# Kernel optimization log

Measured on AMD Instinct MI355X. Metric: run time of the kernel, lower is better.

Reference implementation:

```python
import jax, jax.numpy as jnp
import numpy as np

D_MODEL = 1024
N_HEAD = 16
N_HEAD_MOE = 8
N_EXPERTS = 8
TOP_N = 2
CAP_FACTOR = 1.25
THRESHOLD = 0.2
BAL_COEF = 0.01
Z_COEF = 0.001
B, S = 8, 1024


def setup_inputs() -> dict:
    key = jax.random.key(0)
    ks = jax.random.split(key, 12)
    d, E = D_MODEL, N_EXPERTS
    w = lambda k, shape: jax.random.normal(k, shape, jnp.float32) * 0.02
    return {
        "x": jax.random.normal(ks[0], (B, S, d), jnp.float32),
        "Wq": w(ks[1], (d, d)), "Wk": w(ks[2], (d, d)), "Wv": w(ks[3], (d, d)), "Wo": w(ks[4], (d, d)),
        "bq": jnp.zeros((d,), jnp.float32), "bk": jnp.zeros((d,), jnp.float32),
        "bv": jnp.zeros((d,), jnp.float32), "bo": jnp.zeros((d,), jnp.float32),
        "ln1_g": jnp.ones((d,), jnp.float32), "ln1_b": jnp.zeros((d,), jnp.float32),
        "ln2_g": jnp.ones((d,), jnp.float32), "ln2_b": jnp.zeros((d,), jnp.float32),
        "gate_W": w(ks[5], (d, E)),
        "eWq": w(ks[6], (E, d, d)), "eWk": w(ks[7], (E, d, d)),
        "eWv": w(ks[8], (E, d, d)), "eWo": w(ks[9], (E, d, d)),
    }


def _layernorm(x, g, b, eps=1e-5):
    mu = jnp.mean(x, -1, keepdims=True)
    var = jnp.var(x, -1, keepdims=True)
    return (x - mu) * jax.lax.rsqrt(var + eps) * g + b


def _mha(x, Wq, Wk, Wv, bq, bk, bv, Wo, bo):
    b, s, d = x.shape
    h, hd = N_HEAD, d // N_HEAD
    q = (x @ Wq + bq).reshape(b, s, h, hd)
    k = (x @ Wk + bk).reshape(b, s, h, hd)
    v = (x @ Wv + bv).reshape(b, s, h, hd)
    att = jax.nn.softmax(jnp.einsum('bqhd,bkhd->bhqk', q, k) * (hd ** -0.5), axis=-1)
    o = jnp.einsum('bhqk,bkhd->bqhd', att, v).reshape(b, s, d)
    return o @ Wo + bo


def _moe(x, gate_W, eWq, eWk, eWv, eWo):
    # ST-MoE style top-n routing with capacity dropping; experts are self-attention blocks.
    b, s, d = x.shape
    E = N_EXPERTS
    C = int(S * TOP_N * CAP_FACTOR / E)  # per-expert capacity (per batch row)
    logits = x @ gate_W                      # [b,s,E]
    z_loss = jnp.mean(jnp.square(jax.nn.logsumexp(logits, axis=-1)))
    probs = jax.nn.softmax(logits, axis=-1)
    gates, idxs = jax.lax.top_k(probs, TOP_N)  # [b,s,TOP_N]
    # load-balance loss: E * sum_e (top-1 dispatch fraction) * (mean router prob)
    f = jnp.mean(jax.nn.one_hot(idxs[..., 0], E, dtype=x.dtype), axis=(0, 1))
    P = jnp.mean(probs, axis=(0, 1))
    balance_loss = E * jnp.sum(f * P)

    bb = jnp.broadcast_to(jnp.arange(b)[:, None], (b, s))
    counts = jnp.zeros((b, E), jnp.int32)
    expert_in = jnp.zeros((E, b, C, d), x.dtype)
    slots = []
    for k in range(TOP_N):  # small fixed loop over routing slots
        e_idx = idxs[..., k]
        g = gates[..., k]
        keep_thr = (g > THRESHOLD) if k > 0 else jnp.ones(g.shape, dtype=bool)
        oh = jax.nn.one_hot(e_idx, E, dtype=jnp.int32) * keep_thr[..., None].astype(jnp.int32)
        # exclusive running position within each (batch, expert) buffer
        pos_all = jnp.cumsum(oh, axis=1) - oh + counts[:, None, :]
        pos = jnp.take_along_axis(pos_all, e_idx[..., None], axis=2)[..., 0]
        counts = counts + jnp.sum(oh, axis=1)
        keep = keep_thr & (pos < C)
        p = jnp.clip(pos, 0, C - 1)
        expert_in = expert_in.at[e_idx, bb, p].add(x * keep[..., None].astype(x.dtype))
        slots.append((e_idx, p, keep, g))

    # each expert: multi-head self-attention over its C capacity slots
    h, hd = N_HEAD_MOE, d // N_HEAD_MOE
    q = jnp.einsum('ebcd,edf->ebcf', expert_in, eWq).reshape(E, b, C, h, hd)
    kk = jnp.einsum('ebcd,edf->ebcf', expert_in, eWk).reshape(E, b, C, h, hd)
    v = jnp.einsum('ebcd,edf->ebcf', expert_in, eWv).reshape(E, b, C, h, hd)
    att = jax.nn.softmax(jnp.einsum('ebqhd,ebkhd->ebhqk', q, kk) * (hd ** -0.5), axis=-1)
    o = jnp.einsum('ebhqk,ebkhd->ebqhd', att, v).reshape(E, b, C, d)
    expert_out = jnp.einsum('ebcd,edf->ebcf', o, eWo)

    # combine: gather each token's slot output, weighted by its gate
    y = jnp.zeros_like(x)
    for e_idx, p, keep, g in slots:
        y = y + expert_out[e_idx, bb, p] * (g * keep.astype(x.dtype))[..., None]
    bal = BAL_COEF * balance_loss
    zl = Z_COEF * z_loss
    return y, bal + zl, bal, zl


def reference(x, Wq, Wk, Wv, Wo, bq, bk, bv, bo, ln1_g, ln1_b, ln2_g, ln2_b,
              gate_W, eWq, eWk, eWv, eWo):
    attn = _mha(x, Wq, Wk, Wv, bq, bk, bv, Wo, bo)
    x1 = _layernorm(x + attn, ln1_g, ln1_b)
    moe_out, aux, bal, zl = _moe(x1, gate_W, eWq, eWk, eWv, eWo)
    out = _layernorm(x1 + moe_out, ln2_g, ln2_b)
    return (out, aux, bal, zl)
```

## Files before the change

### kernel.cpp

```cpp
#include <hip/hip_runtime.h>
#include <hip/hip_bf16.h>
#include <math.h>

#define DM    1024
#define NH1   16
#define HDIM1 64
#define NH2   8
#define HDIM2 128
#define NE    8
#define CAPE  320
#define BATCH 8
#define SEQ   1024
#define NTOK  (BATCH*SEQ)
#define OUTN  ((long)NTOK*DM)
#define ECB   ((long)BATCH*CAPE*DM)

typedef short bf16x8 __attribute__((ext_vector_type(8)));
typedef float f32x4  __attribute__((ext_vector_type(4)));

__device__ __forceinline__ unsigned short f2bf(float f) {
    __hip_bfloat16 h = __float2bfloat16(f);
    return *reinterpret_cast<unsigned short*>(&h);
}
__device__ __forceinline__ float bf2f(unsigned short u) {
    unsigned int x = ((unsigned int)u) << 16;
    return __builtin_bit_cast(float, x);
}

__device__ __forceinline__ void async16(const void* g, void* lds) {
    __builtin_amdgcn_global_load_lds(
        (const __attribute__((address_space(1))) unsigned int*)g,
        (__attribute__((address_space(3))) unsigned int*)lds, 16, 0, 0);
}

__device__ __forceinline__ void gemm_core(
    const unsigned short* __restrict__ A, const unsigned short* __restrict__ Bt,
    int m0, int n0, int K, short* ldsA, short* ldsB, f32x4 (&acc)[4][4])
{
    const int t    = threadIdx.x;
    const int lane = t & 63, w = t >> 6;
    const int wr = w >> 1, wc = w & 1;
    const int lq = lane >> 4, lm = lane & 15;
    const int srow = w*16 + (lane >> 2);
    const int skc  = (lane & 3) * 8;
    for (int kb = 0; kb < K; kb += 32) {
        #pragma unroll
        for (int p = 0; p < 2; ++p) {
            async16(A  + (size_t)(m0 + srow + p*64)*K + kb + skc,
                    &ldsA[(w*16 + p*64)*32]);
            async16(Bt + (size_t)(n0 + srow + p*64)*K + kb + skc,
                    &ldsB[(w*16 + p*64)*32]);
        }
        __syncthreads();
        bf16x8 aF[4], bF[4];
        #pragma unroll
        for (int i = 0; i < 4; ++i)
            aF[i] = *(const bf16x8*)&ldsA[(wr*64 + i*16 + lm)*32 + lq*8];
        #pragma unroll
        for (int j = 0; j < 4; ++j)
            bF[j] = *(const bf16x8*)&ldsB[(wc*64 + j*16 + lm)*32 + lq*8];
        #pragma unroll
        for (int i = 0; i < 4; ++i)
            #pragma unroll
            for (int j = 0; j < 4; ++j)
                acc[i][j] = __builtin_amdgcn_mfma_f32_16x16x32_bf16(aF[i], bF[j], acc[i][j], 0, 0, 0);
        __syncthreads();
    }
}

__global__ __launch_bounds__(256) void gemm_bt_f32(
    const unsigned short* __restrict__ A, const unsigned short* __restrict__ Bt,
    const float* __restrict__ bias, float* __restrict__ C, int N, int K)
{
    __shared__ short ldsA[128*32];
    __shared__ short ldsB[128*32];
    const int lane = threadIdx.x & 63, w = threadIdx.x >> 6;
    const int wr = w >> 1, wc = w & 1;
    const int lq = lane >> 4, lm = lane & 15;
    const int m0 = blockIdx.y * 128, n0 = blockIdx.x * 128;
    f32x4 acc[4][4];
    #pragma unroll
    for (int i = 0; i < 4; ++i)
        #pragma unroll
        for (int j = 0; j < 4; ++j) acc[i][j] = (f32x4){0.f,0.f,0.f,0.f};
    gemm_core(A, Bt, m0, n0, K, ldsA, ldsB, acc);
    #pragma unroll
    for (int j = 0; j < 4; ++j) {
        const int gcol = n0 + wc*64 + j*16 + lm;
        const float badd = bias ? bias[gcol] : 0.f;
        #pragma unroll
        for (int i = 0; i < 4; ++i) {
            const int grow = m0 + wr*64 + i*16 + lq*4;
            #pragma unroll
            for (int r = 0; r < 4; ++r)
                C[(size_t)(grow + r)*N + gcol] = acc[i][j][r] + badd;
        }
    }
}

__global__ __launch_bounds__(256) void gemm_qkv(
    const unsigned short* __restrict__ A, const unsigned short* __restrict__ Bt,
    const float* __restrict__ bq, const float* __restrict__ bk, const float* __restrict__ bv,
    unsigned short* __restrict__ C)
{
    __shared__ short ldsA[128*32];
    __shared__ short ldsB[128*32];
    const int lane = threadIdx.x & 63, w = threadIdx.x >> 6;
    const int wr = w >> 1, wc = w & 1;
    const int lq = lane >> 4, lm = lane & 15;
    const int m0 = blockIdx.y * 128, n0g = blockIdx.x * 128;
    const int buf = n0g >> 10;
    const float* bias = (buf == 0) ? bq : (buf == 1) ? bk : bv;
    unsigned short* Cb = C + (size_t)buf * OUTN;
    f32x4 acc[4][4];
    #pragma unroll
    for (int i = 0; i < 4; ++i)
        #pragma unroll
        for (int j = 0; j < 4; ++j) acc[i][j] = (f32x4){0.f,0.f,0.f,0.f};
    gemm_core(A, Bt, m0, n0g, DM, ldsA, ldsB, acc);
    #pragma unroll
    for (int j = 0; j < 4; ++j) {
        const int gcol = (n0g & 1023) + wc*64 + j*16 + lm;
        const float badd = bias[gcol];
        #pragma unroll
        for (int i = 0; i < 4; ++i) {
            const int grow = m0 + wr*64 + i*16 + lq*4;
            #pragma unroll
            for (int r = 0; r < 4; ++r)
                Cb[(size_t)(grow + r)*DM + gcol] = f2bf(acc[i][j][r] + badd);
        }
    }
}

__global__ __launch_bounds__(256) void gemm_eqkv(
    const unsigned short* __restrict__ A,
    const unsigned short* __restrict__ eWTq, const unsigned short* __restrict__ eWTk,
    const unsigned short* __restrict__ eWTv,
    unsigned short* __restrict__ Cq, unsigned short* __restrict__ Ck,
    unsigned short* __restrict__ Cv, int ebase)
{
    __shared__ short ldsA[128*32];
    __shared__ short ldsB[128*32];
    const int lane = threadIdx.x & 63, w = threadIdx.x >> 6;
    const int wr = w >> 1, wc = w & 1;
    const int lq = lane >> 4, lm = lane & 15;
    const int z = blockIdx.z;
    const int eloc = blockIdx.y / 20;
    const unsigned short* Bt =
        ((z == 0) ? eWTq : (z == 1) ? eWTk : eWTv) + (size_t)(ebase + eloc) * (1024l*1024l);
    unsigned short* C = (z == 0) ? Cq : (z == 1) ? Ck : Cv;
    const int m0 = blockIdx.y * 128, n0 = blockIdx.x * 128;
    f32x4 acc[4][4];
    #pragma unroll
    for (int i = 0; i < 4; ++i)
        #pragma unroll
        for (int j = 0; j < 4; ++j) acc[i][j] = (f32x4){0.f,0.f,0.f,0.f};
    gemm_core(A, Bt, m0, n0, DM, ldsA, ldsB, acc);
    #pragma unroll
    for (int j = 0; j < 4; ++j) {
        const int gcol = n0 + wc*64 + j*16 + lm;
        #pragma unroll
        for (int i = 0; i < 4; ++i) {
            const int grow = m0 + wr*64 + i*16 + lq*4;
            #pragma unroll
            for (int r = 0; r < 4; ++r)
                C[(size_t)(grow + r)*DM + gcol] = f2bf(acc[i][j][r]);
        }
    }
}

__global__ __launch_bounds__(256) void gemm_eout(
    const unsigned short* __restrict__ A, const unsigned short* __restrict__ eWTo,
    unsigned short* __restrict__ C, int ebase)
{
    __shared__ short ldsA[128*32];
    __shared__ short ldsB[128*32];
    const int lane = threadIdx.x & 63, w = threadIdx.x >> 6;
    const int wr = w >> 1, wc = w & 1;
    const int lq = lane >> 4, lm = lane & 15;
    const int eloc = blockIdx.y / 20;
    const unsigned short* Bt = eWTo + (size_t)(ebase + eloc) * (1024l*1024l);
    const int m0 = blockIdx.y * 128, n0 = blockIdx.x * 128;
    f32x4 acc[4][4];
    #pragma unroll
    for (int i = 0; i < 4; ++i)
        #pragma unroll
        for (int j = 0; j < 4; ++j) acc[i][j] = (f32x4){0.f,0.f,0.f,0.f};
    gemm_core(A, Bt, m0, n0, DM, ldsA, ldsB, acc);
    #pragma unroll
    for (int j = 0; j < 4; ++j) {
        const int gcol = n0 + wc*64 + j*16 + lm;
        #pragma unroll
        for (int i = 0; i < 4; ++i) {
            const int grow = m0 + wr*64 + i*16 + lq*4;
            #pragma unroll
            for (int r = 0; r < 4; ++r)
                C[(size_t)(grow + r)*DM + gcol] = f2bf(acc[i][j][r]);
        }
    }
}

template<int HD>
__global__ __launch_bounds__(256) void flash_mfma(
    const unsigned short* __restrict__ Q, const unsigned short* __restrict__ K,
    const unsigned short* __restrict__ V, unsigned short* __restrict__ O,
    int rows, float scale)
{
    constexpr int QT = 64, KT = 64;
    constexpr int PADQ = HD + 8;
    constexpr int NKT = HD / 32;
    constexpr int NDT = HD / 16;
    constexpr int CG  = HD / 8;
    constexpr int RPR = 256 / CG;
    constexpr int NP  = KT / RPR;
    __shared__ __align__(16) unsigned short ks[KT * PADQ];
    __shared__ __align__(16) unsigned short vt[HD * KT];
    __shared__ __align__(16) unsigned short pP[4][16 * 72];
    const int t = threadIdx.x, lane = t & 63, w = t >> 6;
    const int lm = lane & 15, quad = lane >> 4;
    const int q0 = blockIdx.x * QT;
    const long base = (long)blockIdx.z * rows * DM + (long)blockIdx.y * HD;
    const int srow = t / CG, scg = t % CG;

    #pragma unroll
    for (int r = 0; r < QT / RPR; ++r) {
        int row = srow + r * RPR;
        *(bf16x8*)&ks[row * PADQ + scg * 8] =
            *(const bf16x8*)&Q[base + (long)(q0 + row) * DM + scg * 8];
    }
    __syncthreads();
    bf16x8 aQ[NKT];
    #pragma unroll
    for (int kk = 0; kk < NKT; ++kk)
        aQ[kk] = *(const bf16x8*)&ks[(w * 16 + lm) * PADQ + kk * 32 + quad * 8];

    float m4[4], l4[4];
    #pragma unroll
    for (int r = 0; r < 4; ++r) { m4[r] = -1e30f; l4[r] = 0.f; }
    f32x4 aco[NDT];
    #pragma unroll
    for (int d = 0; d < NDT; ++d) aco[d] = (f32x4){0.f,0.f,0.f,0.f};

    bf16x8 kr[NP], vr[NP];
    #pragma unroll
    for (int r = 0; r < NP; ++r) {
        int row = srow + r * RPR;
        kr[r] = *(const bf16x8*)&K[base + (long)row * DM + scg * 8];
        vr[r] = *(const bf16x8*)&V[base + (long)row * DM + scg * 8];
    }

    for (int k0 = 0; k0 < rows; k0 += KT) {
        __syncthreads();
        #pragma unroll
        for (int r = 0; r < NP; ++r) {
            int row = srow + r * RPR;
            *(bf16x8*)&ks[row * PADQ + scg * 8] = kr[r];
            #pragma unroll
            for (int u = 0; u < 8; ++u) {
                int d = scg * 8 + u;
                vt[d * KT + ((((row >> 3) ^ (d >> 3) ^ d) & 7)) * 8 + (row & 7)] = ((short*)&vr[r])[u];
            }
        }
        __syncthreads();
        if (k0 + KT < rows) {
            #pragma unroll
            for (int r = 0; r < NP; ++r) {
                int row = srow + r * RPR;
                kr[r] = *(const bf16x8*)&K[base + (long)(k0 + KT + row) * DM + scg * 8];
                vr[r] = *(const bf16x8*)&V[base + (long)(k0 + KT + row) * DM + scg * 8];
            }
        }
        f32x4 sc[4];
        #pragma unroll
        for (int n = 0; n < 4; ++n) {
            f32x4 c = (f32x4){0.f,0.f,0.f,0.f};
            #pragma unroll
            for (int kk = 0; kk < NKT; ++kk) {
                bf16x8 bK = *(const bf16x8*)&ks[(n * 16 + lm) * PADQ + kk * 32 + quad * 8];
                c = __builtin_amdgcn_mfma_f32_16x16x32_bf16(aQ[kk], bK, c, 0, 0, 0);
            }
            #pragma unroll
            for (int r = 0; r < 4; ++r) c[r] *= scale;
            sc[n] = c;
        }
        float alpha[4];
        #pragma unroll
        for (int r = 0; r < 4; ++r) {
            float mx = fmaxf(fmaxf(sc[0][r], sc[1][r]), fmaxf(sc[2][r], sc[3][r]));
            #pragma unroll
            for (int off = 1; off < 16; off <<= 1)
                mx = fmaxf(mx, __shfl_xor(mx, off, 64));
            float mnew = fmaxf(m4[r], mx);
            alpha[r] = __expf(m4[r] - mnew);
            m4[r] = mnew;
            float s = 0.f;
            #pragma unroll
            for (int n = 0; n < 4; ++n) {
                float p = __expf(sc[n][r] - mnew);
                sc[n][r] = p; s += p;
            }
            #pragma unroll
            for (int off = 1; off < 16; off <<= 1)
                s += __shfl_xor(s, off, 64);
            l4[r] = l4[r] * alpha[r] + s;
        }
        #pragma unroll
        for (int n = 0; n < 4; ++n)
            #pragma unroll
            for (int r = 0; r < 4; ++r)
                pP[w][(quad * 4 + r) * 72 + n * 16 + lm] = f2bf(sc[n][r]);
        #pragma unroll
        for (int d = 0; d < NDT; ++d)
            #pragma unroll
            for (int r = 0; r < 4; ++r) aco[d][r] *= alpha[r];
        #pragma unroll
        for (int d = 0; d < NDT; ++d) {
            #pragma unroll
            for (int kk = 0; kk < 2; ++kk) {
                bf16x8 aP = *(const bf16x8*)&pP[w][lm * 72 + kk * 32 + quad * 8];
                int dd = d * 16 + lm;
                int jb = kk * 4 + quad;
                bf16x8 bV = *(const bf16x8*)&vt[dd * KT + (((jb ^ (dd >> 3) ^ dd) & 7) * 8)];
                aco[d] = __builtin_amdgcn_mfma_f32_16x16x32_bf16(aP, bV, aco[d], 0, 0, 0);
            }
        }
    }
    #pragma unroll
    for (int r = 0; r < 4; ++r) l4[r] = 1.f / l4[r];
    #pragma unroll
    for (int d = 0; d < NDT; ++d)
        #pragma unroll
        for (int r = 0; r < 4; ++r)
            O[base + (long)(q0 + w * 16 + quad * 4 + r) * DM + d * 16 + lm] =
                f2bf(aco[d][r] * l4[r]);
}

__global__ __launch_bounds__(256) void transpose_bf16(
    const float* __restrict__ src, unsigned short* __restrict__ dst)
{
    __shared__ float tile[32][33];
    const long mb = (long)blockIdx.z * (1024l*1024l);
    const int tx = threadIdx.x & 31, ty = threadIdx.x >> 5;
    const int r0 = blockIdx.y * 32, c0 = blockIdx.x * 32;
    #pragma unroll
    for (int rr = ty; rr < 32; rr += 8)
        tile[rr][tx] = src[mb + (long)(r0+rr)*1024 + c0 + tx];
    __syncthreads();
    #pragma unroll
    for (int rr = ty; rr < 32; rr += 8)
        dst[mb + (long)(c0+rr)*1024 + r0 + tx] = f2bf(tile[tx][rr]);
}

__global__ __launch_bounds__(256) void convert_bf16(
    const float* __restrict__ src, unsigned short* __restrict__ dst, long n)
{
    long i = ((long)blockIdx.x*256 + threadIdx.x)*4;
    if (i >= n) return;
    float4 v = *(const float4*)&src[i];
    ushort4 o = { f2bf(v.x), f2bf(v.y), f2bf(v.z), f2bf(v.w) };
    *(ushort4*)&dst[i] = o;
}

__global__ __launch_bounds__(256) void ln_residual(
    const float* __restrict__ X, const float* __restrict__ R,
    const float* __restrict__ gam, const float* __restrict__ bet,
    float* __restrict__ Y)
{
    const long row = blockIdx.x;
    const int t = threadIdx.x;
    float4 xv = *(const float4*)&X[row*DM + t*4];
    float4 rv = *(const float4*)&R[row*DM + t*4];
    float v0=xv.x+rv.x, v1=xv.y+rv.y, v2=xv.z+rv.z, v3=xv.w+rv.w;
    float s  = v0+v1+v2+v3;
    float s2 = v0*v0+v1*v1+v2*v2+v3*v3;
    #pragma unroll
    for (int off = 32; off > 0; off >>= 1) {
        s  += __shfl_down(s,  off, 64);
        s2 += __shfl_down(s2, off, 64);
    }
    __shared__ float red[8];
    __shared__ float mv[2];
    const int wid = t >> 6;
    if ((t & 63) == 0) { red[wid] = s; red[4+wid] = s2; }
    __syncthreads();
    if (t == 0) {
        float S  = red[0]+red[1]+red[2]+red[3];
        float S2 = red[4]+red[5]+red[6]+red[7];
        float mean = S * (1.f/DM);
        float var  = S2 * (1.f/DM) - mean*mean;
        mv[0] = mean; mv[1] = rsqrtf(var + 1e-5f);
    }
    __syncthreads();
    float mean = mv[0], inv = mv[1];
    float4 g4 = *(const float4*)&gam[t*4];
    float4 b4 = *(const float4*)&bet[t*4];
    float4 o4;
    o4.x = (v0-mean)*inv*g4.x + b4.x;
    o4.y = (v1-mean)*inv*g4.y + b4.y;
    o4.z = (v2-mean)*inv*g4.z + b4.z;
    o4.w = (v3-mean)*inv*g4.w + b4.w;
    *(float4*)&Y[row*DM + t*4] = o4;
}

__global__ __launch_bounds__(256) void combine_ln(
    const float* __restrict__ X1, const unsigned short* __restrict__ Eout,
    const int* __restrict__ e1, const int* __restrict__ pos1,
    const int* __restrict__ keep1, const float* __restrict__ g1,
    const int* __restrict__ e2, const int* __restrict__ pos2,
    const int* __restrict__ keep2, const float* __restrict__ g2,
    const float* __restrict__ gam, const float* __restrict__ bet,
    float* __restrict__ Y)
{
    const long row = blockIdx.x;
    const int b = (int)(row >> 10);
    const int t = threadIdx.x;
    float4 xv = *(const float4*)&X1[row*DM + t*4];
    float v0=xv.x, v1=xv.y, v2=xv.z, v3=xv.w;
    const float w1 = keep1[row] ? g1[row] : 0.f;
    const float w2 = keep2[row] ? g2[row] : 0.f;
    if (w1 != 0.f) {
        ushort4 u = *(const ushort4*)&Eout[(((size_t)e1[row]*BATCH + b)*CAPE + pos1[row])*DM + t*4];
        v0 += w1*bf2f(u.x); v1 += w1*bf2f(u.y); v2 += w1*bf2f(u.z); v3 += w1*bf2f(u.w);
    }
    if (w2 != 0.f) {
        ushort4 u = *(const ushort4*)&Eout[(((size_t)e2[row]*BATCH + b)*CAPE + pos2[row])*DM + t*4];
        v0 += w2*bf2f(u.x); v1 += w2*bf2f(u.y); v2 += w2*bf2f(u.z); v3 += w2*bf2f(u.w);
    }
    float s  = v0+v1+v2+v3;
    float s2 = v0*v0+v1*v1+v2*v2+v3*v3;
    #pragma unroll
    for (int off = 32; off > 0; off >>= 1) {
        s  += __shfl_down(s,  off, 64);
        s2 += __shfl_down(s2, off, 64);
    }
    __shared__ float red[8];
    __shared__ float mv[2];
    const int wid = t >> 6;
    if ((t & 63) == 0) { red[wid] = s; red[4+wid] = s2; }
    __syncthreads();
    if (t == 0) {
        float S  = red[0]+red[1]+red[2]+red[3];
        float S2 = red[4]+red[5]+red[6]+red[7];
        float mean = S * (1.f/DM);
        float var  = S2 * (1.f/DM) - mean*mean;
        mv[0] = mean; mv[1] = rsqrtf(var + 1e-5f);
    }
    __syncthreads();
    float mean = mv[0], inv = mv[1];
    float4 g4 = *(const float4*)&gam[t*4];
    float4 b4 = *(const float4*)&bet[t*4];
    float4 o4;
    o4.x = (v0-mean)*inv*g4.x + b4.x;
    o4.y = (v1-mean)*inv*g4.y + b4.y;
    o4.z = (v2-mean)*inv*g4.z + b4.z;
    o4.w = (v3-mean)*inv*g4.w + b4.w;
    *(float4*)&Y[row*DM + t*4] = o4;
}

__global__ __launch_bounds__(256) void gate_kernel(
    const float* __restrict__ X1, const float* __restrict__ gW,
    int* __restrict__ e1, int* __restrict__ e2,
    float* __restrict__ g1, float* __restrict__ g2,
    float* __restrict__ accum)
{
    const int t = threadIdx.x, l = t & 63, w = t >> 6;
    const int gwave = blockIdx.x * 4 + w;
    float zacc = 0.f, pacc[8], facc[8];
    #pragma unroll
    for (int e = 0; e < 8; ++e) { pacc[e] = 0.f; facc[e] = 0.f; }

    for (int tok = gwave; tok < NTOK; tok += 2048) {
        const float* xr = X1 + (long)tok*DM;
        float part[8];
        #pragma unroll
        for (int e = 0; e < 8; ++e) part[e] = 0.f;
        #pragma unroll
        for (int pass = 0; pass < 4; ++pass) {
            const int i0 = pass*256 + l*4;
            float4 xv = *(const float4*)&xr[i0];
            const float xs[4] = {xv.x, xv.y, xv.z, xv.w};
            #pragma unroll
            for (int u = 0; u < 4; ++u) {
                float4 w0 = *(const float4*)&gW[(i0+u)*8];
                float4 w1 = *(const float4*)&gW[(i0+u)*8+4];
                part[0]+=xs[u]*w0.x; part[1]+=xs[u]*w0.y; part[2]+=xs[u]*w0.z; part[3]+=xs[u]*w0.w;
                part[4]+=xs[u]*w1.x; part[5]+=xs[u]*w1.y; part[6]+=xs[u]*w1.z; part[7]+=xs[u]*w1.w;
            }
        }
        #pragma unroll
        for (int e = 0; e < 8; ++e) {
            float v = part[e];
            #pragma unroll
            for (int off = 32; off > 0; off >>= 1) v += __shfl_down(v, off, 64);
            part[e] = v;
        }
        if (l == 0) {
            float mx = part[0];
            #pragma unroll
            for (int e = 1; e < 8; ++e) mx = fmaxf(mx, part[e]);
            float p[8]; float sum = 0.f;
            #pragma unroll
            for (int e = 0; e < 8; ++e) { p[e] = __expf(part[e]-mx); sum += p[e]; }
            float lse = mx + __logf(sum);
            float isum = 1.f/sum;
            #pragma unroll
            for (int e = 0; e < 8; ++e) { p[e] *= isum; pacc[e] += p[e]; }
            int b1 = 0;
            #pragma unroll
            for (int e = 1; e < 8; ++e) if (p[e] > p[b1]) b1 = e;
            int b2 = (b1 == 0) ? 1 : 0;
            #pragma unroll
            for (int e = 0; e < 8; ++e) if (e != b1 && e != b2 && p[e] > p[b2]) b2 = e;
            e1[tok] = b1; e2[tok] = b2; g1[tok] = p[b1]; g2[tok] = p[b2];
            zacc += lse*lse;
            facc[b1] += 1.f;
        }
    }
    __shared__ float red[4][17];
    if (l == 0) {
        red[w][0] = zacc;
        #pragma unroll
        for (int e = 0; e < 8; ++e) { red[w][1+e] = pacc[e]; red[w][9+e] = facc[e]; }
    }
    __syncthreads();
    if (t < 17)
        atomicAdd(&accum[t], red[0][t] + red[1][t] + red[2][t] + red[3][t]);
}

__global__ __launch_bounds__(64) void route_scan(
    const int* __restrict__ e1, const int* __restrict__ e2,
    const float* __restrict__ g2,
    int* __restrict__ pos1, int* __restrict__ keep1,
    int* __restrict__ pos2, int* __restrict__ keep2,
    int* __restrict__ slotmap)
{
    const int b = blockIdx.x;
    const int l = threadIdx.x;
    __shared__ int cnt[8];
    if (l < 8) cnt[l] = 0;
    __syncthreads();
    for (int slot = 0; slot < 2; ++slot) {
        const int* eArr = slot ? e2 : e1;
        for (int c = 0; c < SEQ/64; ++c) {
            const int tk = b*SEQ + c*64 + l;
            const int e = eArr[tk];
            const bool valid = slot ? (g2[tk] > 0.2f) : true;
            unsigned long long mymask = 0ull; int addmine = 0;
            #pragma unroll
            for (int ee = 0; ee < 8; ++ee) {
                unsigned long long bm = __ballot(valid && (e == ee));
                if (e == ee) mymask = bm;
                if (l == ee) addmine = (int)__popcll(bm);
            }
            const int p  = cnt[e] + (int)__popcll(mymask & ((1ull << l) - 1ull));
            const int kp = (valid && p < CAPE) ? 1 : 0;
            const int pc = p < CAPE ? p : (CAPE-1);
            if (slot == 0) { pos1[tk] = pc; keep1[tk] = kp; }
            else           { pos2[tk] = pc; keep2[tk] = kp; }
            if (kp) slotmap[(e*BATCH + b)*CAPE + pc] = tk;
            __syncthreads();
            if (l < 8) cnt[l] += addmine;
            __syncthreads();
        }
    }
}

__global__ __launch_bounds__(256) void gather_chunk(
    const float* __restrict__ X1, const int* __restrict__ slotmap,
    unsigned short* __restrict__ Ein, int ebase)
{
    const int slot = blockIdx.x;
    const int t = threadIdx.x;
    const int tok = slotmap[ebase*(BATCH*CAPE) + slot];
    float4 v4 = make_float4(0.f, 0.f, 0.f, 0.f);
    if (tok >= 0) v4 = *(const float4*)&X1[(long)tok*DM + t*4];
    ushort4 o = { f2bf(v4.x), f2bf(v4.y), f2bf(v4.z), f2bf(v4.w) };
    *(ushort4*)&Ein[(long)slot*DM + t*4] = o;
}

__global__ void finalize_loss(const float* __restrict__ accum, float* __restrict__ out)
{
    float z = accum[0] * (1.0f/NTOK);
    float s = 0.f;
    for (int e = 0; e < 8; ++e)
        s += (accum[1+e] * (1.0f/NTOK)) * (accum[9+e] * (1.0f/NTOK));
    float bal = 0.01f * 8.0f * s;
    float zl  = 0.001f * z;
    out[OUTN]   = bal + zl;
    out[OUTN+1] = bal;
    out[OUTN+2] = zl;
}

extern "C" void kernel_launch(void* const* d_in, const int* in_sizes, int n_in,
                              void* d_out, int out_size, void* d_ws, size_t ws_size,
                              hipStream_t stream)
{
    (void)in_sizes; (void)n_in; (void)out_size; (void)ws_size;
    const float* x    = (const float*)d_in[0];
    const float* Wq   = (const float*)d_in[1];
    const float* Wk   = (const float*)d_in[2];
    const float* Wv   = (const float*)d_in[3];
    const float* Wo   = (const float*)d_in[4];
    const float* bq   = (const float*)d_in[5];
    const float* bk   = (const float*)d_in[6];
    const float* bv   = (const float*)d_in[7];
    const float* bo   = (const float*)d_in[8];
    const float* ln1g = (const float*)d_in[9];
    const float* ln1b = (const float*)d_in[10];
    const float* ln2g = (const float*)d_in[11];
    const float* ln2b = (const float*)d_in[12];
    const float* gW   = (const float*)d_in[13];
    const float* eWq  = (const float*)d_in[14];
    const float* eWk  = (const float*)d_in[15];
    const float* eWv  = (const float*)d_in[16];
    const float* eWo  = (const float*)d_in[17];
    float* out = (float*)d_out;

    char* ws = (char*)d_ws;
    const size_t MB = 1048576;
    const long MATE = 1024l*1024l;
    unsigned short* WTq  = (unsigned short*)(ws);
    unsigned short* WTk  = WTq + 1*MATE;
    unsigned short* WTv  = WTq + 2*MATE;
    unsigned short* WTo  = WTq + 3*MATE;
    unsigned short* eWTq = WTq + 4*MATE;
    unsigned short* eWTk = WTq + 12*MATE;
    unsigned short* eWTv = WTq + 20*MATE;
    unsigned short* eWTo = WTq + 28*MATE;
    int*   e1i   = (int*)(ws + 72*MB);
    int*   e2i   = e1i + NTOK;
    int*   pos1  = e1i + 2*NTOK;
    int*   pos2  = e1i + 3*NTOK;
    int*   keep1 = e1i + 4*NTOK;
    int*   keep2 = e1i + 5*NTOK;
    int*   slotmap = e1i + 6*NTOK;
    float* g1f   = (float*)(e1i + 6*NTOK + NE*BATCH*CAPE);
    float* g2f   = g1f + NTOK;
    float* accum = g2f + NTOK;
    unsigned short* xb = (unsigned short*)(ws + 74*MB);
    unsigned short* ob = (unsigned short*)(ws + 90*MB);
    unsigned short* Qb = (unsigned short*)(ws + 106*MB);
    float* Pf = (float*)(ws + 106*MB);
    float* x1 = (float*)(ws + 154*MB);
    unsigned short* eoutAll = (unsigned short*)(ws + 74*MB);
    unsigned short* Einb = (unsigned short*)(ws + 114*MB);
    unsigned short* eqb  = (unsigned short*)(ws + 124*MB);
    unsigned short* ekb  = (unsigned short*)(ws + 134*MB);
    unsigned short* evb  = (unsigned short*)(ws + 144*MB);
    unsigned short* eob  = Einb;

    dim3 blk(256);
    dim3 tgrid(32, 32, 1), tgrid8(32, 32, 8);

    transpose_bf16<<<tgrid,  blk, 0, stream>>>(Wq,  WTq);
    transpose_bf16<<<tgrid,  blk, 0, stream>>>(Wk,  WTk);
    transpose_bf16<<<tgrid,  blk, 0, stream>>>(Wv,  WTv);
    transpose_bf16<<<tgrid,  blk, 0, stream>>>(Wo,  WTo);
    transpose_bf16<<<tgrid8, blk, 0, stream>>>(eWq, eWTq);
    transpose_bf16<<<tgrid8, blk, 0, stream>>>(eWk, eWTk);
    transpose_bf16<<<tgrid8, blk, 0, stream>>>(eWv, eWTv);
    transpose_bf16<<<tgrid8, blk, 0, stream>>>(eWo, eWTo);
    convert_bf16<<<NTOK, blk, 0, stream>>>(x, xb, OUTN);

    gemm_qkv<<<dim3(3*DM/128, NTOK/128), blk, 0, stream>>>(xb, WTq, bq, bk, bv, Qb);
    flash_mfma<HDIM1><<<dim3(SEQ/64, NH1, BATCH), blk, 0, stream>>>(
        Qb, Qb + OUTN, Qb + 2*OUTN, ob, SEQ, 0.125f);
    gemm_bt_f32<<<dim3(DM/128, NTOK/128), blk, 0, stream>>>(ob, WTo, bo, Pf, DM, DM);
    ln_residual<<<NTOK, blk, 0, stream>>>(x, Pf, ln1g, ln1b, x1);

    hipMemsetAsync(accum, 0, 17*sizeof(float), stream);
    hipMemsetAsync(slotmap, 0xFF, NE*BATCH*CAPE*sizeof(int), stream);
    gate_kernel<<<512, blk, 0, stream>>>(x1, gW, e1i, e2i, g1f, g2f, accum);
    route_scan<<<BATCH, dim3(64), 0, stream>>>(e1i, e2i, g2f, pos1, keep1, pos2, keep2, slotmap);

    for (int c = 0; c < 4; ++c) {
        const int ebase = c*2;
        gather_chunk<<<2*BATCH*CAPE, blk, 0, stream>>>(x1, slotmap, Einb, ebase);
        gemm_eqkv<<<dim3(DM/128, 2*BATCH*CAPE/128, 3), blk, 0, stream>>>(
            Einb, eWTq, eWTk, eWTv, eqb, ekb, evb, ebase);
        flash_mfma<HDIM2><<<dim3(CAPE/64, NH2, 2*BATCH), blk, 0, stream>>>(
            eqb, ekb, evb, eob, CAPE, 0.088388347648318447f);
        gemm_eout<<<dim3(DM/128, 2*BATCH*CAPE/128), blk, 0, stream>>>(
            eob, eWTo, eoutAll + (size_t)ebase*ECB, ebase);
    }

    combine_ln<<<NTOK, blk, 0, stream>>>(x1, eoutAll, e1i, pos1, keep1, g1f,
                                         e2i, pos2, keep2, g2f, ln2g, ln2b, out);
    finalize_loss<<<1, 1, 0, stream>>>(accum, out);
}
```

Before: 1.030 ms.

## Process two query sub-tiles per flash block to reuse staged K/V tiles

The flash attention kernel is templated on a number of 64-row query sub-tiles per block. The first attention call uses two sub-tiles, so each K/V tile loaded and transposed into shared memory serves 128 query rows. This halves global K/V traffic and staging work per query row for the 16-head attention, at the cost of more registers per thread and half as many blocks. The P staging stride also changes from 72 to 76 to alter the LDS bank mapping.

```diff
diff --git a/kernel.cpp b/kernel.cpp
--- a/kernel.cpp
+++ b/kernel.cpp
@@ -200,46 +200,54 @@
     }
 }
 
-template<int HD>
+template<int HD, int NS>
 __global__ __launch_bounds__(256) void flash_mfma(
     const unsigned short* __restrict__ Q, const unsigned short* __restrict__ K,
     const unsigned short* __restrict__ V, unsigned short* __restrict__ O,
     int rows, float scale)
 {
-    constexpr int QT = 64, KT = 64;
+    constexpr int KT = 64;
     constexpr int PADQ = HD + 8;
     constexpr int NKT = HD / 32;
     constexpr int NDT = HD / 16;
     constexpr int CG  = HD / 8;
     constexpr int RPR = 256 / CG;
     constexpr int NP  = KT / RPR;
+    constexpr int PST = 76;
     __shared__ __align__(16) unsigned short ks[KT * PADQ];
     __shared__ __align__(16) unsigned short vt[HD * KT];
-    __shared__ __align__(16) unsigned short pP[4][16 * 72];
+    __shared__ __align__(16) unsigned short pP[4][16 * PST];
     const int t = threadIdx.x, lane = t & 63, w = t >> 6;
     const int lm = lane & 15, quad = lane >> 4;
-    const int q0 = blockIdx.x * QT;
+    const int q0 = blockIdx.x * (64 * NS);
     const long base = (long)blockIdx.z * rows * DM + (long)blockIdx.y * HD;
     const int srow = t / CG, scg = t % CG;
 
-    #pragma unroll
-    for (int r = 0; r < QT / RPR; ++r) {
-        int row = srow + r * RPR;
-        *(bf16x8*)&ks[row * PADQ + scg * 8] =
-            *(const bf16x8*)&Q[base + (long)(q0 + row) * DM + scg * 8];
-    }
-    __syncthreads();
-    bf16x8 aQ[NKT];
-    #pragma unroll
-    for (int kk = 0; kk < NKT; ++kk)
-        aQ[kk] = *(const bf16x8*)&ks[(w * 16 + lm) * PADQ + kk * 32 + quad * 8];
-
-    float m4[4], l4[4];
-    #pragma unroll
-    for (int r = 0; r < 4; ++r) { m4[r] = -1e30f; l4[r] = 0.f; }
-    f32x4 aco[NDT];
-    #pragma unroll
-    for (int d = 0; d < NDT; ++d) aco[d] = (f32x4){0.f,0.f,0.f,0.f};
+    bf16x8 aQ[NS][NKT];
+    #pragma unroll
+    for (int s = 0; s < NS; ++s) {
+        if (s) __syncthreads();
+        #pragma unroll
+        for (int r = 0; r < 64 / RPR; ++r) {
+            int row = srow + r * RPR;
+            *(bf16x8*)&ks[row * PADQ + scg * 8] =
+                *(const bf16x8*)&Q[base + (long)(q0 + s * 64 + row) * DM + scg * 8];
+        }
+        __syncthreads();
+        #pragma unroll
+        for (int kk = 0; kk < NKT; ++kk)
+            aQ[s][kk] = *(const bf16x8*)&ks[(w * 16 + lm) * PADQ + kk * 32 + quad * 8];
+    }
+
+    float m4[NS][4], l4[NS][4];
+    f32x4 aco[NS][NDT];
+    #pragma unroll
+    for (int s = 0; s < NS; ++s) {
+        #pragma unroll
+        for (int r = 0; r < 4; ++r) { m4[s][r] = -1e30f; l4[s][r] = 0.f; }
+        #pragma unroll
+        for (int d = 0; d < NDT; ++d) aco[s][d] = (f32x4){0.f,0.f,0.f,0.f};
+    }
 
     bf16x8 kr[NP], vr[NP];
     #pragma unroll
@@ -270,69 +278,74 @@
                 vr[r] = *(const bf16x8*)&V[base + (long)(k0 + KT + row) * DM + scg * 8];
             }
         }
-        f32x4 sc[4];
-        #pragma unroll
-        for (int n = 0; n < 4; ++n) {
-            f32x4 c = (f32x4){0.f,0.f,0.f,0.f};
-            #pragma unroll
-            for (int kk = 0; kk < NKT; ++kk) {
-                bf16x8 bK = *(const bf16x8*)&ks[(n * 16 + lm) * PADQ + kk * 32 + quad * 8];
-                c = __builtin_amdgcn_mfma_f32_16x16x32_bf16(aQ[kk], bK, c, 0, 0, 0);
+        #pragma unroll
+        for (int s = 0; s < NS; ++s) {
+            f32x4 sc[4];
+            #pragma unroll
+            for (int n = 0; n < 4; ++n) {
+                f32x4 c = (f32x4){0.f,0.f,0.f,0.f};
+                #pragma unroll
+                for (int kk = 0; kk < NKT; ++kk) {
+                    bf16x8 bK = *(const bf16x8*)&ks[(n * 16 + lm) * PADQ + kk * 32 + quad * 8];
+                    c = __builtin_amdgcn_mfma_f32_16x16x32_bf16(aQ[s][kk], bK, c, 0, 0, 0);
+                }
+                #pragma unroll
+                for (int r = 0; r < 4; ++r) c[r] *= scale;
+                sc[n] = c;
             }
-            #pragma unroll
-            for (int r = 0; r < 4; ++r) c[r] *= scale;
-            sc[n] = c;
-        }
-        float alpha[4];
+            float alpha[4];
+            #pragma unroll
+            for (int r = 0; r < 4; ++r) {
+                float mx = fmaxf(fmaxf(sc[0][r], sc[1][r]), fmaxf(sc[2][r], sc[3][r]));
+                #pragma unroll
+                for (int off = 1; off < 16; off <<= 1)
+                    mx = fmaxf(mx, __shfl_xor(mx, off, 64));
+                float mnew = fmaxf(m4[s][r], mx);
+                alpha[r] = __expf(m4[s][r] - mnew);
+                m4[s][r] = mnew;
+                float sum = 0.f;
+                #pragma unroll
+                for (int n = 0; n < 4; ++n) {
+                    float p = __expf(sc[n][r] - mnew);
+                    sc[n][r] = p; sum += p;
+                }
+                #pragma unroll
+                for (int off = 1; off < 16; off <<= 1)
+                    sum += __shfl_xor(sum, off, 64);
+                l4[s][r] = l4[s][r] * alpha[r] + sum;
+            }
+            #pragma unroll
+            for (int n = 0; n < 4; ++n)
+                #pragma unroll
+                for (int r = 0; r < 4; ++r)
+                    pP[w][(quad * 4 + r) * PST + n * 16 + lm] = f2bf(sc[n][r]);
+            #pragma unroll
+            for (int d = 0; d < NDT; ++d)
+                #pragma unroll
+                for (int r = 0; r < 4; ++r) aco[s][d][r] *= alpha[r];
+            #pragma unroll
+            for (int d = 0; d < NDT; ++d) {
+                #pragma unroll
+                for (int kk = 0; kk < 2; ++kk) {
+                    bf16x8 aP = *(const bf16x8*)&pP[w][lm * PST + kk * 32 + quad * 8];
+                    int dd = d * 16 + lm;
+                    int jb = kk * 4 + quad;
+                    bf16x8 bV = *(const bf16x8*)&vt[dd * KT + (((jb ^ (dd >> 3) ^ dd) & 7) * 8)];
+                    aco[s][d] = __builtin_amdgcn_mfma_f32_16x16x32_bf16(aP, bV, aco[s][d], 0, 0, 0);
+                }
+            }
+        }
+    }
+    #pragma unroll
+    for (int s = 0; s < NS; ++s)
         #pragma unroll
         for (int r = 0; r < 4; ++r) {
-            float mx = fmaxf(fmaxf(sc[0][r], sc[1][r]), fmaxf(sc[2][r], sc[3][r]));
-            #pragma unroll
-            for (int off = 1; off < 16; off <<= 1)
-                mx = fmaxf(mx, __shfl_xor(mx, off, 64));
-            float mnew = fmaxf(m4[r], mx);
-            alpha[r] = __expf(m4[r] - mnew);
-            m4[r] = mnew;
-            float s = 0.f;
-            #pragma unroll
-            for (int n = 0; n < 4; ++n) {
-                float p = __expf(sc[n][r] - mnew);
-                sc[n][r] = p; s += p;
-            }
-            #pragma unroll
-            for (int off = 1; off < 16; off <<= 1)
-                s += __shfl_xor(s, off, 64);
-            l4[r] = l4[r] * alpha[r] + s;
-        }
-        #pragma unroll
-        for (int n = 0; n < 4; ++n)
-            #pragma unroll
-            for (int r = 0; r < 4; ++r)
-                pP[w][(quad * 4 + r) * 72 + n * 16 + lm] = f2bf(sc[n][r]);
-        #pragma unroll
-        for (int d = 0; d < NDT; ++d)
-            #pragma unroll
-            for (int r = 0; r < 4; ++r) aco[d][r] *= alpha[r];
-        #pragma unroll
-        for (int d = 0; d < NDT; ++d) {
-            #pragma unroll
-            for (int kk = 0; kk < 2; ++kk) {
-                bf16x8 aP = *(const bf16x8*)&pP[w][lm * 72 + kk * 32 + quad * 8];
-                int dd = d * 16 + lm;
-                int jb = kk * 4 + quad;
-                bf16x8 bV = *(const bf16x8*)&vt[dd * KT + (((jb ^ (dd >> 3) ^ dd) & 7) * 8)];
-                aco[d] = __builtin_amdgcn_mfma_f32_16x16x32_bf16(aP, bV, aco[d], 0, 0, 0);
-            }
-        }
-    }
-    #pragma unroll
-    for (int r = 0; r < 4; ++r) l4[r] = 1.f / l4[r];
-    #pragma unroll
-    for (int d = 0; d < NDT; ++d)
-        #pragma unroll
-        for (int r = 0; r < 4; ++r)
-            O[base + (long)(q0 + w * 16 + quad * 4 + r) * DM + d * 16 + lm] =
-                f2bf(aco[d][r] * l4[r]);
+            float inv = 1.f / l4[s][r];
+            #pragma unroll
+            for (int d = 0; d < NDT; ++d)
+                O[base + (long)(q0 + s * 64 + w * 16 + quad * 4 + r) * DM + d * 16 + lm] =
+                    f2bf(aco[s][d][r] * inv);
+        }
 }
 
 __global__ __launch_bounds__(256) void transpose_bf16(
@@ -663,7 +676,7 @@
     convert_bf16<<<NTOK, blk, 0, stream>>>(x, xb, OUTN);
 
     gemm_qkv<<<dim3(3*DM/128, NTOK/128), blk, 0, stream>>>(xb, WTq, bq, bk, bv, Qb);
-    flash_mfma<HDIM1><<<dim3(SEQ/64, NH1, BATCH), blk, 0, stream>>>(
+    flash_mfma<HDIM1,2><<<dim3(SEQ/128, NH1, BATCH), blk, 0, stream>>>(
         Qb, Qb + OUTN, Qb + 2*OUTN, ob, SEQ, 0.125f);
     gemm_bt_f32<<<dim3(DM/128, NTOK/128), blk, 0, stream>>>(ob, WTo, bo, Pf, DM, DM);
     ln_residual<<<NTOK, blk, 0, stream>>>(x, Pf, ln1g, ln1b, x1);
@@ -678,7 +691,7 @@
         gather_chunk<<<2*BATCH*CAPE, blk, 0, stream>>>(x1, slotmap, Einb, ebase);
         gemm_eqkv<<<dim3(DM/128, 2*BATCH*CAPE/128, 3), blk, 0, stream>>>(
             Einb, eWTq, eWTk, eWTv, eqb, ekb, evb, ebase);
-        flash_mfma<HDIM2><<<dim3(CAPE/64, NH2, 2*BATCH), blk, 0, stream>>>(
+        flash_mfma<HDIM2,1><<<dim3(CAPE/64, NH2, 2*BATCH), blk, 0, stream>>>(
             eqb, ekb, evb, eob, CAPE, 0.088388347648318447f);
         gemm_eout<<<dim3(DM/128, 2*BATCH*CAPE/128), blk, 0, stream>>>(
             eob, eWTo, eoutAll + (size_t)ebase*ECB, ebase);
```

After: 1.027 ms. No clear change (-0.3%).
